# Kernel optimization log

Measured on AMD Instinct MI355X. Metric: run time of the kernel, lower is better.

The kernel has to match this reference:

```python
import jax, jax.numpy as jnp
import numpy as np
import math

B, TQ, TK, D, I, H = 2, 2048, 2048, 2048, 2048, 16
HD = I // H  # head dim = 128
PAD = 128    # trailing keys treated as padding


def setup_inputs() -> dict:
    key = jax.random.key(0)
    ks = jax.random.split(key, 12)
    s_in = 1.0 / math.sqrt(D)
    s_i = 1.0 / math.sqrt(I)
    inp = {
        "query_states": jax.random.normal(ks[0], (B, TQ, D), jnp.float32),
        "kv_states": jax.random.normal(ks[1], (B, TK, D), jnp.float32),
        # pad the trailing PAD key positions (True = masked out)
        "kv_padding_mask": jnp.broadcast_to(jnp.arange(TK) >= (TK - PAD), (B, TK)),
        "Wq": jax.random.normal(ks[2], (I, D), jnp.float32) * s_in,
        "bq": jnp.zeros((I,), jnp.float32),
        "Wk": jax.random.normal(ks[3], (I, D), jnp.float32) * s_in,
        "bk": jnp.zeros((I,), jnp.float32),
        "Wv": jax.random.normal(ks[4], (I, D), jnp.float32) * s_in,
        "bv": jnp.zeros((I,), jnp.float32),
        "Wo": jax.random.normal(ks[5], (D, I), jnp.float32) * s_i,
        "bo": jnp.zeros((D,), jnp.float32),
        "gate": jnp.zeros((D,), jnp.float32),
    }
    return inp


def _split_heads(x):
    b, t, _ = x.shape
    return x.reshape(b, t, H, HD).transpose(0, 2, 1, 3)  # (B,H,T,HD)


def reference(query_states, kv_states, kv_padding_mask, Wq, bq, Wk, bk, Wv, bv, Wo, bo, gate):
    q = _split_heads(query_states @ Wq.T + bq)  # (B,H,Tq,HD)
    k = _split_heads(kv_states @ Wk.T + bk)     # (B,H,Tk,HD)
    v = _split_heads(kv_states @ Wv.T + bv)     # (B,H,Tk,HD)

    scores = jnp.einsum("bhqd,bhkd->bhqk", q, k) / jnp.sqrt(jnp.float32(HD))
    causal = jnp.triu(jnp.ones((TQ, TK), bool), k=1)  # True above diagonal
    neg_inf = jnp.float32(-jnp.inf)
    scores = jnp.where(causal[None, None, :, :], neg_inf, scores)
    scores = jnp.where(kv_padding_mask[:, None, None, :], neg_inf, scores)

    probs = jax.nn.softmax(scores, axis=-1)  # dropout p=0 -> identity
    ctx = jnp.einsum("bhqk,bhkd->bhqd", probs, v)
    ctx = ctx.transpose(0, 2, 1, 3).reshape(B, TQ, I)  # merge heads
    ctx = ctx @ Wo.T + bo
    ctx = ctx * jax.nn.sigmoid(gate)  # gated residual, gate init 0 -> 0.5
    return query_states + ctx
```

## Files before the change

### kernel.cpp

```cpp
#include <hip/hip_runtime.h>
#include <hip/hip_bf16.h>
#include <stdint.h>

#define B_N   2
#define T_Q   2048
#define T_K   2048
#define D_IN  2048
#define I_IN  2048
#define H_N   16
#define HD_N  128

using bf16 = __hip_bfloat16;
typedef short bf16x8 __attribute__((ext_vector_type(8)));
typedef float floatx4 __attribute__((ext_vector_type(4)));

__device__ __forceinline__ void async_copy16(const void* gsrc, void* ldst) {
    __builtin_amdgcn_global_load_lds(
        (const __attribute__((address_space(1))) void*)gsrc,
        (__attribute__((address_space(3))) void*)ldst, 16, 0, 0);
}

__device__ __forceinline__ floatx4 mfma_bf16(bf16x8 a, bf16x8 b, floatx4 c) {
    return __builtin_amdgcn_mfma_f32_16x16x32_bf16(a, b, c, 0, 0, 0);
}

#define XG 1048576
#define WG 524288
struct CastArgs {
    const float *s0, *s1, *s2, *s3, *s4, *s5;
    bf16 *d0, *d1, *d2, *d3, *d4, *d5;
};
__global__ void cast_all(CastArgs a) {
    int g = blockIdx.x * 256 + threadIdx.x;
    const float* src; bf16* dst; size_t off;
    if (g < XG)            { src = a.s0; dst = a.d0; off = (size_t)g * 8; }
    else if (g < 2 * XG)   { src = a.s1; dst = a.d1; off = (size_t)(g - XG) * 8; }
    else {
        int r = g - 2 * XG, s = r >> 19;
        off = (size_t)(r & (WG - 1)) * 8;
        src = (s == 0) ? a.s2 : (s == 1) ? a.s3 : (s == 2) ? a.s4 : a.s5;
        dst = (s == 0) ? a.d2 : (s == 1) ? a.d3 : (s == 2) ? a.d4 : a.d5;
    }
    float4 x = *((const float4*)(src + off));
    float4 y = *((const float4*)(src + off + 4));
    union { bf16x8 v; bf16 h[8]; } u;
    u.h[0] = __float2bfloat16(x.x); u.h[1] = __float2bfloat16(x.y);
    u.h[2] = __float2bfloat16(x.z); u.h[3] = __float2bfloat16(x.w);
    u.h[4] = __float2bfloat16(y.x); u.h[5] = __float2bfloat16(y.y);
    u.h[6] = __float2bfloat16(y.z); u.h[7] = __float2bfloat16(y.w);
    *((bf16x8*)(dst + off)) = u.v;
}

__global__ __launch_bounds__(256, 1) void qkv_gemm(
    const bf16* __restrict__ xq, const bf16* __restrict__ xkv,
    const bf16* __restrict__ wq, const bf16* __restrict__ wk, const bf16* __restrict__ wv,
    const float* __restrict__ bq, const float* __restrict__ bk, const float* __restrict__ bv,
    bf16* __restrict__ qo, bf16* __restrict__ ko, bf16* __restrict__ vt)
{
    __shared__ bf16 sA[128 * 32];
    __shared__ bf16 sB[128 * 32];
    const int tid  = threadIdx.x;
    const int wave = tid >> 6, lane = tid & 63;
    const int quad = lane >> 4, r16 = lane & 15;
    const int wy = wave >> 1, wx = wave & 1;
    const int m0 = blockIdx.x * 128;
    const int seg = blockIdx.y >> 4;
    const int n0 = (blockIdx.y & 15) * 128;
    const int K = D_IN;

    const bf16* A = (seg == 0) ? xq : xkv;
    const bf16* W = (seg == 0) ? wq : (seg == 1) ? wk : wv;
    const float* bias = (seg == 0) ? bq : (seg == 1) ? bk : bv;

    floatx4 acc[4][4];
    #pragma unroll
    for (int i = 0; i < 4; i++)
        #pragma unroll
        for (int j = 0; j < 4; j++) acc[i][j] = (floatx4)(0.0f);

    const int ca0 = wave*128 + lane;
    const int ca1 = ca0 + 64;
    const int ra0 = ca0 >> 2, ga0c = ((ca0 & 3) ^ (ra0 & 3) ^ ((ra0 >> 2) & 3)) * 8;
    const int ra1 = ca1 >> 2, ga1c = ((ca1 & 3) ^ (ra1 & 3) ^ ((ra1 >> 2) & 3)) * 8;
    const bf16* gA0 = A + (size_t)(m0 + ra0)*K + ga0c;
    const bf16* gA1 = A + (size_t)(m0 + ra1)*K + ga1c;
    const bf16* gB0 = W + (size_t)(n0 + ra0)*K + ga0c;
    const bf16* gB1 = W + (size_t)(n0 + ra1)*K + ga1c;
    bf16* lA0 = &sA[ca0*8]; bf16* lA1 = &sA[ca1*8];
    bf16* lB0 = &sB[ca0*8]; bf16* lB1 = &sB[ca1*8];

    for (int k0 = 0; k0 < K; k0 += 32) {
        __syncthreads();
        async_copy16(gA0 + k0, lA0);
        async_copy16(gA1 + k0, lA1);
        async_copy16(gB0 + k0, lB0);
        async_copy16(gB1 + k0, lB1);
        __syncthreads();

        bf16x8 af[4], bw[4];
        #pragma unroll
        for (int mt = 0; mt < 4; mt++) {
            int r  = wy*64 + mt*16 + r16;
            int cc = quad ^ (r & 3) ^ ((r >> 2) & 3);
            af[mt] = *(const bf16x8*)(&sA[r*32 + cc*8]);
        }
        #pragma unroll
        for (int nt = 0; nt < 4; nt++) {
            int r  = wx*64 + nt*16 + r16;
            int cc = quad ^ (r & 3) ^ ((r >> 2) & 3);
            bw[nt] = *(const bf16x8*)(&sB[r*32 + cc*8]);
        }
        #pragma unroll
        for (int mt = 0; mt < 4; mt++)
            #pragma unroll
            for (int nt = 0; nt < 4; nt++)
                acc[mt][nt] = mfma_bf16(af[mt], bw[nt], acc[mt][nt]);
    }

    bf16* Cb = (seg == 0) ? qo : ko;
    #pragma unroll
    for (int mt = 0; mt < 4; mt++)
        #pragma unroll
        for (int nt = 0; nt < 4; nt++) {
            int col = n0 + wx*64 + nt*16 + r16;
            float bs = bias[col];
            if (seg < 2) {
                #pragma unroll
                for (int r = 0; r < 4; r++) {
                    size_t row = (size_t)(m0 + wy*64 + mt*16 + quad*4 + r);
                    Cb[row*I_IN + col] = __float2bfloat16(acc[mt][nt][r] + bs);
                }
            } else {
                int hh = col >> 7, dd = col & 127;
                int m  = m0 + wy*64 + mt*16 + quad*4;
                int bb = m >> 11, tt = m & 2047;
                union { ushort4 u; bf16 h[4]; } pk;
                #pragma unroll
                for (int r = 0; r < 4; r++) pk.h[r] = __float2bfloat16(acc[mt][nt][r] + bs);
                *((ushort4*)(vt + ((size_t)((bb*16 + hh)*128 + dd))*T_K + tt)) = pk.u;
            }
        }
}

__global__ __launch_bounds__(256, 2) void flash_attn(
    const bf16* __restrict__ Q,
    const bf16* __restrict__ Km,
    const bf16* __restrict__ Vt,
    bf16* __restrict__ Ctx)
{
    __shared__ bf16 sK[2][64 * 128];
    __shared__ bf16 sV[2][128 * 64];
    __shared__ bf16 sP[64 * 80];

    const int tid  = threadIdx.x;
    const int wave = tid >> 6, lane = tid & 63;
    const int quad = lane >> 4, r16 = lane & 15;
    const int n  = blockIdx.x;
    const int bh = n & 31, qt = 31 - (n >> 5);
    const int b  = bh >> 4, h = bh & 15;

    const bf16* Qbase = Q + ((size_t)(b*T_Q) + qt*64 + wave*16) * I_IN + h*HD_N;
    bf16x8 qf[4];
    #pragma unroll
    for (int ks = 0; ks < 4; ks++)
        qf[ks] = *(const bf16x8*)(Qbase + (size_t)r16*I_IN + ks*32 + quad*8);

    floatx4 acc_o[8];
    #pragma unroll
    for (int nt = 0; nt < 8; nt++) acc_o[nt] = (floatx4)(0.0f);
    float m2[4], l[4];
    #pragma unroll
    for (int r = 0; r < 4; r++) { m2[r] = -3.0e38f; l[r] = 0.0f; }

    const int kend = (qt < 29) ? qt : 29;
    const bf16* Kb0 = Km + (size_t)(b*T_K) * I_IN + h*HD_N;
    const bf16* Vb0 = Vt + (size_t)bh * HD_N * T_K;
    const float c1 = 0.08838834764831845f * 1.4426950408889634f;

    {
        #pragma unroll
        for (int i = 0; i < 4; i++) {
            int c = wave*256 + i*64 + lane;
            int row = c >> 4, cc = (c & 15) ^ (row & 15);
            async_copy16(Kb0 + (size_t)row*I_IN + cc*8, &sK[0][c*8]);
        }
        #pragma unroll
        for (int i = 0; i < 4; i++) {
            int c = wave*256 + i*64 + lane;
            int row = c >> 3, cc = (c & 7) ^ (row & 7);
            async_copy16(Vb0 + (size_t)row*T_K + cc*8, &sV[0][c*8]);
        }
    }

    for (int kt = 0; kt <= kend; kt++) {
        const int cur = kt & 1;
        if (kt < kend) {
            const int nxt = cur ^ 1;
            #pragma unroll
            for (int i = 0; i < 4; i++) {
                int c = wave*256 + i*64 + lane;
                int row = c >> 4, cc = (c & 15) ^ (row & 15);
                async_copy16(Kb0 + (size_t)((kt+1)*64 + row)*I_IN + cc*8, &sK[nxt][c*8]);
            }
            #pragma unroll
            for (int i = 0; i < 4; i++) {
                int c = wave*256 + i*64 + lane;
                int row = c >> 3, cc = (c & 7) ^ (row & 7);
                async_copy16(Vb0 + (size_t)row*T_K + (kt+1)*64 + cc*8, &sV[nxt][c*8]);
            }
            asm volatile("s_waitcnt vmcnt(8)\n\ts_barrier" ::: "memory");
        } else {
            asm volatile("s_waitcnt vmcnt(0)\n\ts_barrier" ::: "memory");
        }

        floatx4 sacc[4];
        #pragma unroll
        for (int nt = 0; nt < 4; nt++) sacc[nt] = (floatx4)(0.0f);
        #pragma unroll
        for (int ks = 0; ks < 4; ks++) {
            bf16x8 bk[4];
            #pragma unroll
            for (int nt = 0; nt < 4; nt++) {
                int key = nt*16 + r16;
                int cc  = (ks*4 + quad) ^ r16;
                bk[nt] = *(const bf16x8*)(&sK[cur][key*128 + cc*8]);
            }
            #pragma unroll
            for (int nt = 0; nt < 4; nt++)
                sacc[nt] = mfma_bf16(qf[ks], bk[nt], sacc[nt]);
        }

        const bool diag = (kt == qt);
        float tv[4][4];
        #pragma unroll
        for (int nt = 0; nt < 4; nt++)
            #pragma unroll
            for (int r = 0; r < 4; r++) {
                float v = sacc[nt][r] * c1;
                if (diag && (nt*16 + r16 > wave*16 + quad*4 + r)) v = -1.0e30f;
                tv[nt][r] = v;
            }

        #pragma unroll
        for (int r = 0; r < 4; r++) {
            float mx = tv[0][r];
            #pragma unroll
            for (int nt = 1; nt < 4; nt++) mx = fmaxf(mx, tv[nt][r]);
            mx = fmaxf(mx, __shfl_xor(mx, 1, 64));
            mx = fmaxf(mx, __shfl_xor(mx, 2, 64));
            mx = fmaxf(mx, __shfl_xor(mx, 4, 64));
            mx = fmaxf(mx, __shfl_xor(mx, 8, 64));
            float mn = fmaxf(m2[r], mx);
            float alpha = exp2f(m2[r] - mn);
            m2[r] = mn;
            float rs = 0.0f;
            int prow = wave*16 + quad*4 + r;
            #pragma unroll
            for (int nt = 0; nt < 4; nt++) {
                float p = exp2f(tv[nt][r] - mn);
                rs += p;
                sP[prow*80 + nt*16 + r16] = __float2bfloat16(p);
            }
            rs += __shfl_xor(rs, 1, 64);
            rs += __shfl_xor(rs, 2, 64);
            rs += __shfl_xor(rs, 4, 64);
            rs += __shfl_xor(rs, 8, 64);
            l[r] = l[r]*alpha + rs;
            #pragma unroll
            for (int nt = 0; nt < 8; nt++) acc_o[nt][r] *= alpha;
        }

        #pragma unroll
        for (int ks2 = 0; ks2 < 2; ks2++) {
            bf16x8 ap = *(const bf16x8*)(&sP[(wave*16 + r16)*80 + ks2*32 + quad*8]);
            #pragma unroll
            for (int nt = 0; nt < 8; nt++) {
                int d  = nt*16 + r16;
                int cc = (ks2*4 + quad) ^ (d & 7);
                bf16x8 bv = *(const bf16x8*)(&sV[cur][d*64 + cc*8]);
                acc_o[nt] = mfma_bf16(ap, bv, acc_o[nt]);
            }
        }

        asm volatile("s_waitcnt lgkmcnt(0)\n\ts_barrier" ::: "memory");
    }

    bf16* Cb = Ctx + ((size_t)(b*T_Q) + qt*64 + wave*16) * I_IN + h*HD_N;
    #pragma unroll
    for (int r = 0; r < 4; r++) {
        float inv = 1.0f / l[r];
        #pragma unroll
        for (int nt = 0; nt < 8; nt++)
            Cb[(size_t)(quad*4 + r)*I_IN + nt*16 + r16] =
                __float2bfloat16(acc_o[nt][r] * inv);
    }
}

__global__ __launch_bounds__(256, 1) void gemm_final(
    const bf16* __restrict__ A, const bf16* __restrict__ W,
    const float* __restrict__ bias, const float* __restrict__ gate,
    const float* __restrict__ resid, float* __restrict__ Cf)
{
    __shared__ bf16 sA[128 * 32];
    __shared__ bf16 sB[128 * 32];
    const int tid  = threadIdx.x;
    const int wave = tid >> 6, lane = tid & 63;
    const int quad = lane >> 4, r16 = lane & 15;
    const int wy = wave >> 1, wx = wave & 1;
    const int m0 = blockIdx.x * 128;
    const int n0 = blockIdx.y * 128;
    const int K = I_IN, N = D_IN;

    floatx4 acc[4][4];
    #pragma unroll
    for (int i = 0; i < 4; i++)
        #pragma unroll
        for (int j = 0; j < 4; j++) acc[i][j] = (floatx4)(0.0f);

    const int ca0 = wave*128 + lane;
    const int ca1 = ca0 + 64;
    const int ra0 = ca0 >> 2, ga0c = ((ca0 & 3) ^ (ra0 & 3) ^ ((ra0 >> 2) & 3)) * 8;
    const int ra1 = ca1 >> 2, ga1c = ((ca1 & 3) ^ (ra1 & 3) ^ ((ra1 >> 2) & 3)) * 8;
    const bf16* gA0 = A + (size_t)(m0 + ra0)*K + ga0c;
    const bf16* gA1 = A + (size_t)(m0 + ra1)*K + ga1c;
    const bf16* gB0 = W + (size_t)(n0 + ra0)*K + ga0c;
    const bf16* gB1 = W + (size_t)(n0 + ra1)*K + ga1c;
    bf16* lA0 = &sA[ca0*8]; bf16* lA1 = &sA[ca1*8];
    bf16* lB0 = &sB[ca0*8]; bf16* lB1 = &sB[ca1*8];

    for (int k0 = 0; k0 < K; k0 += 32) {
        __syncthreads();
        async_copy16(gA0 + k0, lA0);
        async_copy16(gA1 + k0, lA1);
        async_copy16(gB0 + k0, lB0);
        async_copy16(gB1 + k0, lB1);
        __syncthreads();

        bf16x8 af[4], bw[4];
        #pragma unroll
        for (int mt = 0; mt < 4; mt++) {
            int r  = wy*64 + mt*16 + r16;
            int cc = quad ^ (r & 3) ^ ((r >> 2) & 3);
            af[mt] = *(const bf16x8*)(&sA[r*32 + cc*8]);
        }
        #pragma unroll
        for (int nt = 0; nt < 4; nt++) {
            int r  = wx*64 + nt*16 + r16;
            int cc = quad ^ (r & 3) ^ ((r >> 2) & 3);
            bw[nt] = *(const bf16x8*)(&sB[r*32 + cc*8]);
        }
        #pragma unroll
        for (int mt = 0; mt < 4; mt++)
            #pragma unroll
            for (int nt = 0; nt < 4; nt++)
                acc[mt][nt] = mfma_bf16(af[mt], bw[nt], acc[mt][nt]);
    }

    #pragma unroll
    for (int mt = 0; mt < 4; mt++)
        #pragma unroll
        for (int nt = 0; nt < 4; nt++) {
            int col = n0 + wx*64 + nt*16 + r16;
            float bs = bias[col];
            float g  = gate[col];
            float sg = 1.0f / (1.0f + exp2f(-g * 1.4426950408889634f));
            #pragma unroll
            for (int r = 0; r < 4; r++) {
                size_t row = (size_t)(m0 + wy*64 + mt*16 + quad*4 + r);
                Cf[row*N + col] = resid[row*N + col] + sg * (acc[mt][nt][r] + bs);
            }
        }
}

extern "C" void kernel_launch(void* const* d_in, const int* in_sizes, int n_in,
                              void* d_out, int out_size, void* d_ws, size_t ws_size,
                              hipStream_t stream)
{
    const float* qs   = (const float*)d_in[0];
    const float* kvs  = (const float*)d_in[1];
    const float* Wq   = (const float*)d_in[3];
    const float* bq   = (const float*)d_in[4];
    const float* Wk   = (const float*)d_in[5];
    const float* bk   = (const float*)d_in[6];
    const float* Wv   = (const float*)d_in[7];
    const float* bv   = (const float*)d_in[8];
    const float* Wo   = (const float*)d_in[9];
    const float* bo   = (const float*)d_in[10];
    const float* gate = (const float*)d_in[11];
    float* out = (float*)d_out;

    bf16* ws = (bf16*)d_ws;
    const size_t WSZ = (size_t)I_IN * D_IN;
    const size_t XSZ = (size_t)B_N * T_Q * D_IN;
    bf16* wq_b  = ws;
    bf16* wk_b  = wq_b + WSZ;
    bf16* wv_b  = wk_b + WSZ;
    bf16* wo_b  = wv_b + WSZ;
    bf16* xq_b  = wo_b + WSZ;
    bf16* xkv_b = xq_b + XSZ;
    bf16* q_b   = xkv_b + XSZ;
    bf16* k_b   = q_b + XSZ;
    bf16* vt_b  = k_b + XSZ;
    bf16* ctx_b = xq_b;

    CastArgs ca;
    ca.s0 = qs;  ca.d0 = xq_b;
    ca.s1 = kvs; ca.d1 = xkv_b;
    ca.s2 = Wq;  ca.d2 = wq_b;
    ca.s3 = Wk;  ca.d3 = wk_b;
    ca.s4 = Wv;  ca.d4 = wv_b;
    ca.s5 = Wo;  ca.d5 = wo_b;
    cast_all<<<16384, 256, 0, stream>>>(ca);

    qkv_gemm<<<dim3(32, 48), 256, 0, stream>>>(xq_b, xkv_b, wq_b, wk_b, wv_b,
                                               bq, bk, bv, q_b, k_b, vt_b);

    flash_attn<<<1024, 256, 0, stream>>>(q_b, k_b, vt_b, ctx_b);

    gemm_final<<<dim3(32, 16), 256, 0, stream>>>(ctx_b, wo_b, bo, gate, qs, out);
}
```

Before: 432.8 us.

## Double-buffer GEMM K loops and transpose attention score layout with LDS-staged output

```diff
diff --git a/kernel.cpp b/kernel.cpp
--- a/kernel.cpp
+++ b/kernel.cpp
@@ -57,8 +57,8 @@
     const float* __restrict__ bq, const float* __restrict__ bk, const float* __restrict__ bv,
     bf16* __restrict__ qo, bf16* __restrict__ ko, bf16* __restrict__ vt)
 {
-    __shared__ bf16 sA[128 * 32];
-    __shared__ bf16 sB[128 * 32];
+    __shared__ bf16 sA[2][128 * 32];
+    __shared__ bf16 sB[2][128 * 32];
     const int tid  = threadIdx.x;
     const int wave = tid >> 6, lane = tid & 63;
     const int quad = lane >> 4, r16 = lane & 15;
@@ -86,35 +86,46 @@
     const bf16* gA1 = A + (size_t)(m0 + ra1)*K + ga1c;
     const bf16* gB0 = W + (size_t)(n0 + ra0)*K + ga0c;
     const bf16* gB1 = W + (size_t)(n0 + ra1)*K + ga1c;
-    bf16* lA0 = &sA[ca0*8]; bf16* lA1 = &sA[ca1*8];
-    bf16* lB0 = &sB[ca0*8]; bf16* lB1 = &sB[ca1*8];
-
-    for (int k0 = 0; k0 < K; k0 += 32) {
-        __syncthreads();
-        async_copy16(gA0 + k0, lA0);
-        async_copy16(gA1 + k0, lA1);
-        async_copy16(gB0 + k0, lB0);
-        async_copy16(gB1 + k0, lB1);
-        __syncthreads();
+
+    async_copy16(gA0, &sA[0][ca0*8]);
+    async_copy16(gA1, &sA[0][ca1*8]);
+    async_copy16(gB0, &sB[0][ca0*8]);
+    async_copy16(gB1, &sB[0][ca1*8]);
+
+    for (int it = 0; it < 64; it++) {
+        const int cur = it & 1;
+        if (it < 63) {
+            const int nxt = cur ^ 1;
+            const int k0 = (it + 1) * 32;
+            async_copy16(gA0 + k0, &sA[nxt][ca0*8]);
+            async_copy16(gA1 + k0, &sA[nxt][ca1*8]);
+            async_copy16(gB0 + k0, &sB[nxt][ca0*8]);
+            async_copy16(gB1 + k0, &sB[nxt][ca1*8]);
+            asm volatile("s_waitcnt vmcnt(4)\n\ts_barrier" ::: "memory");
+        } else {
+            asm volatile("s_waitcnt vmcnt(0)\n\ts_barrier" ::: "memory");
+        }
 
         bf16x8 af[4], bw[4];
         #pragma unroll
         for (int mt = 0; mt < 4; mt++) {
             int r  = wy*64 + mt*16 + r16;
             int cc = quad ^ (r & 3) ^ ((r >> 2) & 3);
-            af[mt] = *(const bf16x8*)(&sA[r*32 + cc*8]);
+            af[mt] = *(const bf16x8*)(&sA[cur][r*32 + cc*8]);
         }
         #pragma unroll
         for (int nt = 0; nt < 4; nt++) {
             int r  = wx*64 + nt*16 + r16;
             int cc = quad ^ (r & 3) ^ ((r >> 2) & 3);
-            bw[nt] = *(const bf16x8*)(&sB[r*32 + cc*8]);
+            bw[nt] = *(const bf16x8*)(&sB[cur][r*32 + cc*8]);
         }
         #pragma unroll
         for (int mt = 0; mt < 4; mt++)
             #pragma unroll
             for (int nt = 0; nt < 4; nt++)
                 acc[mt][nt] = mfma_bf16(af[mt], bw[nt], acc[mt][nt]);
+
+        asm volatile("s_waitcnt lgkmcnt(0)\n\ts_barrier" ::: "memory");
     }
 
     bf16* Cb = (seg == 0) ? qo : ko;
@@ -150,7 +161,7 @@
 {
     __shared__ bf16 sK[2][64 * 128];
     __shared__ bf16 sV[2][128 * 64];
-    __shared__ bf16 sP[64 * 80];
+    __shared__ bf16 sPT[64 * 72];
 
     const int tid  = threadIdx.x;
     const int wave = tid >> 6, lane = tid & 63;
@@ -158,6 +169,7 @@
     const int n  = blockIdx.x;
     const int bh = n & 31, qt = 31 - (n >> 5);
     const int b  = bh >> 4, h = bh & 15;
+    const int q_row = wave*16 + r16;
 
     const bf16* Qbase = Q + ((size_t)(b*T_Q) + qt*64 + wave*16) * I_IN + h*HD_N;
     bf16x8 qf[4];
@@ -168,9 +180,7 @@
     floatx4 acc_o[8];
     #pragma unroll
     for (int nt = 0; nt < 8; nt++) acc_o[nt] = (floatx4)(0.0f);
-    float m2[4], l[4];
-    #pragma unroll
-    for (int r = 0; r < 4; r++) { m2[r] = -3.0e38f; l[r] = 0.0f; }
+    float m2 = -3.0e38f, l = 0.0f;
 
     const int kend = (qt < 29) ? qt : 29;
     const bf16* Kb0 = Km + (size_t)(b*T_K) * I_IN + h*HD_N;
@@ -213,86 +223,96 @@
             asm volatile("s_waitcnt vmcnt(0)\n\ts_barrier" ::: "memory");
         }
 
-        floatx4 sacc[4];
-        #pragma unroll
-        for (int nt = 0; nt < 4; nt++) sacc[nt] = (floatx4)(0.0f);
+        floatx4 st[4];
+        #pragma unroll
+        for (int t = 0; t < 4; t++) st[t] = (floatx4)(0.0f);
         #pragma unroll
         for (int ks = 0; ks < 4; ks++) {
-            bf16x8 bk[4];
-            #pragma unroll
-            for (int nt = 0; nt < 4; nt++) {
-                int key = nt*16 + r16;
+            bf16x8 kf[4];
+            #pragma unroll
+            for (int t = 0; t < 4; t++) {
+                int key = t*16 + r16;
                 int cc  = (ks*4 + quad) ^ r16;
-                bk[nt] = *(const bf16x8*)(&sK[cur][key*128 + cc*8]);
-            }
-            #pragma unroll
-            for (int nt = 0; nt < 4; nt++)
-                sacc[nt] = mfma_bf16(qf[ks], bk[nt], sacc[nt]);
+                kf[t] = *(const bf16x8*)(&sK[cur][key*128 + cc*8]);
+            }
+            #pragma unroll
+            for (int t = 0; t < 4; t++)
+                st[t] = mfma_bf16(kf[t], qf[ks], st[t]);
         }
 
         const bool diag = (kt == qt);
         float tv[4][4];
         #pragma unroll
-        for (int nt = 0; nt < 4; nt++)
+        for (int t = 0; t < 4; t++)
             #pragma unroll
             for (int r = 0; r < 4; r++) {
-                float v = sacc[nt][r] * c1;
-                if (diag && (nt*16 + r16 > wave*16 + quad*4 + r)) v = -1.0e30f;
-                tv[nt][r] = v;
-            }
-
-        #pragma unroll
-        for (int r = 0; r < 4; r++) {
-            float mx = tv[0][r];
-            #pragma unroll
-            for (int nt = 1; nt < 4; nt++) mx = fmaxf(mx, tv[nt][r]);
-            mx = fmaxf(mx, __shfl_xor(mx, 1, 64));
-            mx = fmaxf(mx, __shfl_xor(mx, 2, 64));
-            mx = fmaxf(mx, __shfl_xor(mx, 4, 64));
-            mx = fmaxf(mx, __shfl_xor(mx, 8, 64));
-            float mn = fmaxf(m2[r], mx);
-            float alpha = exp2f(m2[r] - mn);
-            m2[r] = mn;
-            float rs = 0.0f;
-            int prow = wave*16 + quad*4 + r;
-            #pragma unroll
-            for (int nt = 0; nt < 4; nt++) {
-                float p = exp2f(tv[nt][r] - mn);
+                float v = st[t][r] * c1;
+                if (diag && (t*16 + quad*4 + r > q_row)) v = -1.0e30f;
+                tv[t][r] = v;
+            }
+
+        float mx = tv[0][0];
+        #pragma unroll
+        for (int t = 0; t < 4; t++)
+            #pragma unroll
+            for (int r = 0; r < 4; r++) mx = fmaxf(mx, tv[t][r]);
+        mx = fmaxf(mx, __shfl_xor(mx, 16, 64));
+        mx = fmaxf(mx, __shfl_xor(mx, 32, 64));
+        float mn = fmaxf(m2, mx);
+        float alpha = exp2f(m2 - mn);
+        m2 = mn;
+        float rs = 0.0f;
+        #pragma unroll
+        for (int t = 0; t < 4; t++) {
+            union { uint2 u2; bf16 hh[4]; } w;
+            #pragma unroll
+            for (int r = 0; r < 4; r++) {
+                float p = exp2f(tv[t][r] - mn);
                 rs += p;
-                sP[prow*80 + nt*16 + r16] = __float2bfloat16(p);
-            }
-            rs += __shfl_xor(rs, 1, 64);
-            rs += __shfl_xor(rs, 2, 64);
-            rs += __shfl_xor(rs, 4, 64);
-            rs += __shfl_xor(rs, 8, 64);
-            l[r] = l[r]*alpha + rs;
-            #pragma unroll
-            for (int nt = 0; nt < 8; nt++) acc_o[nt][r] *= alpha;
-        }
+                w.hh[r] = __float2bfloat16(p);
+            }
+            *((uint2*)(&sPT[q_row*72 + t*16 + quad*4])) = w.u2;
+        }
+        rs += __shfl_xor(rs, 16, 64);
+        rs += __shfl_xor(rs, 32, 64);
+        l = l*alpha + rs;
+        #pragma unroll
+        for (int nt = 0; nt < 8; nt++)
+            #pragma unroll
+            for (int r = 0; r < 4; r++) acc_o[nt][r] *= alpha;
 
         #pragma unroll
         for (int ks2 = 0; ks2 < 2; ks2++) {
-            bf16x8 ap = *(const bf16x8*)(&sP[(wave*16 + r16)*80 + ks2*32 + quad*8]);
+            bf16x8 pb = *(const bf16x8*)(&sPT[q_row*72 + ks2*32 + quad*8]);
             #pragma unroll
             for (int nt = 0; nt < 8; nt++) {
                 int d  = nt*16 + r16;
                 int cc = (ks2*4 + quad) ^ (d & 7);
-                bf16x8 bv = *(const bf16x8*)(&sV[cur][d*64 + cc*8]);
-                acc_o[nt] = mfma_bf16(ap, bv, acc_o[nt]);
+                bf16x8 vf = *(const bf16x8*)(&sV[cur][d*64 + cc*8]);
+                acc_o[nt] = mfma_bf16(vf, pb, acc_o[nt]);
             }
         }
 
         asm volatile("s_waitcnt lgkmcnt(0)\n\ts_barrier" ::: "memory");
     }
 
-    bf16* Cb = Ctx + ((size_t)(b*T_Q) + qt*64 + wave*16) * I_IN + h*HD_N;
-    #pragma unroll
-    for (int r = 0; r < 4; r++) {
-        float inv = 1.0f / l[r];
-        #pragma unroll
-        for (int nt = 0; nt < 8; nt++)
-            Cb[(size_t)(quad*4 + r)*I_IN + nt*16 + r16] =
-                __float2bfloat16(acc_o[nt][r] * inv);
+    float inv = 1.0f / l;
+    bf16* scr = (bf16*)&sK[0][0];
+    __syncthreads();
+    #pragma unroll
+    for (int nt = 0; nt < 8; nt++) {
+        union { uint2 u2; bf16 hh[4]; } w;
+        #pragma unroll
+        for (int r = 0; r < 4; r++) w.hh[r] = __float2bfloat16(acc_o[nt][r] * inv);
+        *((uint2*)(&scr[q_row*136 + nt*16 + quad*4])) = w.u2;
+    }
+    __syncthreads();
+    bf16* Cb = Ctx + ((size_t)(b*T_Q) + qt*64) * I_IN + h*HD_N;
+    #pragma unroll
+    for (int i = 0; i < 4; i++) {
+        int row = wave*16 + i*4 + quad;
+        bf16x8 v = *(const bf16x8*)(&scr[row*136 + r16*8]);
+        *((bf16x8*)(Cb + (size_t)row*I_IN + r16*8)) = v;
     }
 }
 
@@ -301,8 +321,8 @@
     const float* __restrict__ bias, const float* __restrict__ gate,
     const float* __restrict__ resid, float* __restrict__ Cf)
 {
-    __shared__ bf16 sA[128 * 32];
-    __shared__ bf16 sB[128 * 32];
+    __shared__ bf16 sA[2][128 * 32];
+    __shared__ bf16 sB[2][128 * 32];
     const int tid  = threadIdx.x;
     const int wave = tid >> 6, lane = tid & 63;
     const int quad = lane >> 4, r16 = lane & 15;
@@ -325,35 +345,46 @@
     const bf16* gA1 = A + (size_t)(m0 + ra1)*K + ga1c;
     const bf16* gB0 = W + (size_t)(n0 + ra0)*K + ga0c;
     const bf16* gB1 = W + (size_t)(n0 + ra1)*K + ga1c;
-    bf16* lA0 = &sA[ca0*8]; bf16* lA1 = &sA[ca1*8];
-    bf16* lB0 = &sB[ca0*8]; bf16* lB1 = &sB[ca1*8];
-
-    for (int k0 = 0; k0 < K; k0 += 32) {
-        __syncthreads();
-        async_copy16(gA0 + k0, lA0);
-        async_copy16(gA1 + k0, lA1);
-        async_copy16(gB0 + k0, lB0);
-        async_copy16(gB1 + k0, lB1);
-        __syncthreads();
+
+    async_copy16(gA0, &sA[0][ca0*8]);
+    async_copy16(gA1, &sA[0][ca1*8]);
+    async_copy16(gB0, &sB[0][ca0*8]);
+    async_copy16(gB1, &sB[0][ca1*8]);
+
+    for (int it = 0; it < 64; it++) {
+        const int cur = it & 1;
+        if (it < 63) {
+            const int nxt = cur ^ 1;
+            const int k0 = (it + 1) * 32;
+            async_copy16(gA0 + k0, &sA[nxt][ca0*8]);
+            async_copy16(gA1 + k0, &sA[nxt][ca1*8]);
+            async_copy16(gB0 + k0, &sB[nxt][ca0*8]);
+            async_copy16(gB1 + k0, &sB[nxt][ca1*8]);
+            asm volatile("s_waitcnt vmcnt(4)\n\ts_barrier" ::: "memory");
+        } else {
+            asm volatile("s_waitcnt vmcnt(0)\n\ts_barrier" ::: "memory");
+        }
 
         bf16x8 af[4], bw[4];
         #pragma unroll
         for (int mt = 0; mt < 4; mt++) {
             int r  = wy*64 + mt*16 + r16;
             int cc = quad ^ (r & 3) ^ ((r >> 2) & 3);
-            af[mt] = *(const bf16x8*)(&sA[r*32 + cc*8]);
+            af[mt] = *(const bf16x8*)(&sA[cur][r*32 + cc*8]);
         }
         #pragma unroll
         for (int nt = 0; nt < 4; nt++) {
             int r  = wx*64 + nt*16 + r16;
             int cc = quad ^ (r & 3) ^ ((r >> 2) & 3);
-            bw[nt] = *(const bf16x8*)(&sB[r*32 + cc*8]);
+            bw[nt] = *(const bf16x8*)(&sB[cur][r*32 + cc*8]);
         }
         #pragma unroll
         for (int mt = 0; mt < 4; mt++)
             #pragma unroll
             for (int nt = 0; nt < 4; nt++)
                 acc[mt][nt] = mfma_bf16(af[mt], bw[nt], acc[mt][nt]);
+
+        asm volatile("s_waitcnt lgkmcnt(0)\n\ts_barrier" ::: "memory");
     }
 
     #pragma unroll
```

New measurement: 438.3 us. Within noise of the previous version (+1.3%).
